# Kernel optimization log

Hardware: AMD Instinct MI355X
Metric: run time of the kernel (lower is better)

## Reference

```python
import jax, jax.numpy as jnp
import numpy as np


def _gelu(x):
    # torch F.gelu default = exact (erf) gelu
    return jax.nn.gelu(x, approximate=False)


def _gatv2(x, src, dst, Wl, bl, Wr, br, att, bout, n):
    """PyG GATv2Conv, concat=False (mean over heads), negative_slope=0.2."""
    H, C = att.shape
    xl = (x @ Wl + bl).reshape(n, H, C)  # source-side transform (messages)
    xr = (x @ Wr + br).reshape(n, H, C)  # target-side transform
    e = jax.nn.leaky_relu(xl[src] + xr[dst], 0.2)      # [E,H,C]
    logits = jnp.einsum('ehc,hc->eh', e, att)          # [E,H]
    # segment softmax over incoming edges of each target node
    m = jax.ops.segment_max(logits, dst, num_segments=n)
    m = jnp.where(jnp.isfinite(m), m, 0.0)
    p = jnp.exp(logits - m[dst])
    den = jax.ops.segment_sum(p, dst, num_segments=n)
    alpha = p / (den[dst] + 1e-16)
    out = jax.ops.segment_sum(alpha[:, :, None] * xl[src], dst, num_segments=n)  # [N,H,C]
    return out.mean(axis=1) + bout


def _gnorm(x, w, b, ms):
    """PyG GraphNorm with a single graph (batch == zeros)."""
    mu = x.mean(axis=0, keepdims=True)
    o = x - ms * mu
    var = (o * o).mean(axis=0, keepdims=True)
    return w * o / jnp.sqrt(var + 1e-5) + b


def setup_inputs() -> dict:
    N, E, HID, LAT = 50000, 300000, 128, 256
    key = jax.random.key(0)
    ks = iter(jax.random.split(key, 48))

    def rn(shape, s=0.05):
        return jax.random.normal(next(ks), shape, jnp.float32) * s

    d = {}
    d['z_g'] = rn((1, LAT), 1.0)
    d['edge_index'] = jax.random.randint(next(ks), (2, E), 0, N, dtype=jnp.int32)
    d['template_vertices'] = rn((N, 3), 1.0)
    d['W_ne1'] = rn((3, HID)); d['b_ne1'] = jnp.zeros((HID,))
    d['W_ne2'] = rn((HID, HID)); d['b_ne2'] = jnp.zeros((HID,))
    d['W_s1'] = rn((LAT, HID)); d['b_s1'] = jnp.zeros((HID,))
    d['W_s2'] = rn((HID, HID)); d['b_s2'] = jnp.zeros((HID,))
    for i, h in ((1, 2), (2, 2), (3, 1)):
        d[f'Wl{i}'] = rn((HID, h * HID)); d[f'bl{i}'] = jnp.zeros((h * HID,))
        d[f'Wr{i}'] = rn((HID, h * HID)); d[f'br{i}'] = jnp.zeros((h * HID,))
        d[f'att{i}'] = rn((h, HID)); d[f'bo{i}'] = jnp.zeros((HID,))
        d[f'gn{i}_w'] = jnp.ones((HID,)); d[f'gn{i}_b'] = jnp.zeros((HID,))
        d[f'gn{i}_ms'] = jnp.ones((HID,))
    d['W_h1'] = rn((HID, HID // 2)); d['b_h1'] = jnp.zeros((HID // 2,))
    d['W_h2'] = rn((HID // 2, 3)); d['b_h2'] = jnp.zeros((3,))
    return d


def reference(z_g, edge_index, template_vertices,
              W_ne1, b_ne1, W_ne2, b_ne2, W_s1, b_s1, W_s2, b_s2,
              Wl1, bl1, Wr1, br1, att1, bo1, gn1_w, gn1_b, gn1_ms,
              Wl2, bl2, Wr2, br2, att2, bo2, gn2_w, gn2_b, gn2_ms,
              Wl3, bl3, Wr3, br3, att3, bo3, gn3_w, gn3_b, gn3_ms,
              W_h1, b_h1, W_h2, b_h2):
    n = template_vertices.shape[0]
    sl = jnp.arange(n, dtype=edge_index.dtype)
    src = jnp.concatenate([edge_index[0], sl])  # GATv2Conv add_self_loops=True
    dst = jnp.concatenate([edge_index[1], sl])
    # node embedding + broadcast style (eval mode -> dropout is identity)
    x = _gelu(template_vertices @ W_ne1 + b_ne1) @ W_ne2 + b_ne2
    style = _gelu(z_g @ W_s1 + b_s1) @ W_s2 + b_s2   # [1, hidden]
    x = x + style
    x = _gelu(_gnorm(_gatv2(x, src, dst, Wl1, bl1, Wr1, br1, att1, bo1, n), gn1_w, gn1_b, gn1_ms))
    x = _gelu(_gnorm(_gatv2(x, src, dst, Wl2, bl2, Wr2, br2, att2, bo2, n), gn2_w, gn2_b, gn2_ms))
    x = _gelu(_gnorm(_gatv2(x, src, dst, Wl3, bl3, Wr3, br3, att3, bo3, n), gn3_w, gn3_b, gn3_ms))
    displacement = _gelu(x @ W_h1 + b_h1) @ W_h2 + b_h2   # [n, 3]
    return displacement
```

## Files before the change

### kernel.cpp

```cpp
#include <hip/hip_runtime.h>
#include <hip/hip_fp16.h>
#include <math.h>

#define DEVINL __device__ __forceinline__

using bf16x8 = __attribute__((ext_vector_type(8))) short;
using f32x4  = __attribute__((ext_vector_type(4))) float;
using u16x4  = __attribute__((ext_vector_type(4))) unsigned short;
using f16x2  = __attribute__((ext_vector_type(2))) _Float16;

DEVINL float gelu_f(float v) { return 0.5f * v * (1.0f + erff(v * 0.7071067811865475f)); }
DEVINL unsigned short f2bf(float f) {
    union { float f; unsigned u; } c; c.f = f;
    unsigned r = c.u + 0x7fffu + ((c.u >> 16) & 1u);
    return (unsigned short)(r >> 16);
}
DEVINL float bf2f(unsigned short s) {
    union { unsigned u; float f; } c; c.u = (unsigned)s << 16;
    return c.f;
}
DEVINL unsigned short f2h(float f) {
    __half h = __float2half_rn(f);
    return *(unsigned short*)&h;
}
DEVINL f16x2 b2h2(unsigned u) {
    union { unsigned u; f16x2 h; } c; c.u = u; return c.h;
}
DEVINL void gl_lds16(const void* g, void* l) {
    __builtin_amdgcn_global_load_lds(
        (const __attribute__((address_space(1))) unsigned*)g,
        (__attribute__((address_space(3))) unsigned*)l, 16, 0, 0);
}

__global__ void style_k(const float* __restrict__ zg, const float* __restrict__ W1,
                        const float* __restrict__ b1, const float* __restrict__ W2,
                        const float* __restrict__ b2, float* __restrict__ style) {
    __shared__ float s1[128];
    int j = threadIdx.x;
    float a = b1[j];
    for (int k = 0; k < 256; k++) a = fmaf(zg[k], W1[k * 128 + j], a);
    s1[j] = gelu_f(a);
    __syncthreads();
    float o = b2[j];
    for (int k = 0; k < 128; k++) o = fmaf(s1[k], W2[k * 128 + j], o);
    style[j] = o;
}

__global__ void ne1_k(const float* __restrict__ tv, const float* __restrict__ W,
                      const float* __restrict__ b, float* __restrict__ h1,
                      int* __restrict__ counts, int Nn) {
    int idx = blockIdx.x * blockDim.x + threadIdx.x;
    if (idx < Nn) counts[idx] = 0;
    if (idx >= Nn * 128) return;
    int n = idx >> 7, c = idx & 127;
    float o = fmaf(tv[n * 3 + 0], W[c],
              fmaf(tv[n * 3 + 1], W[128 + c],
              fmaf(tv[n * 3 + 2], W[256 + c], b[c])));
    h1[idx] = gelu_f(o);
}

struct PrepArgs {
    const float* src[8];
    unsigned short* dst;
    int dstoff[8];
    int off[9];
    int shift[8];
};
__global__ void prep_k(PrepArgs a) {
    int idx = blockIdx.x * 256 + threadIdx.x;
    if (idx >= a.off[8]) return;
    int s = 0;
    while (idx >= a.off[s + 1]) s++;
    int e = idx - a.off[s];
    int sh = a.shift[s];
    int k = e >> sh, j = e & ((1 << sh) - 1);
    float w = a.src[s][e];
    unsigned short hi = f2bf(w);
    unsigned short lo = f2bf(w - bf2f(hi));
    int c = j >> 4, lr = j & 15;
    int s2 = k >> 5, lk = (k >> 3) & 3, i = k & 7;
    int lane = lk * 16 + lr;
    size_t base = (size_t)a.dstoff[s] + (size_t)c * 4096 + s2 * 512 + lane * 8 + i;
    a.dst[base] = hi;
    a.dst[base + 2048] = lo;
}

template <int OUT, int EPI, bool DUAL, typename OutT, int PRE, int SPLIT>
__global__ __launch_bounds__(256) void mfma_lin_k(
    const float* __restrict__ xin,
    const unsigned short* __restrict__ WT0, const float* __restrict__ b0,
    const unsigned short* __restrict__ WT1, const float* __restrict__ b1,
    const float* __restrict__ style, const float* __restrict__ AB,
    OutT* __restrict__ out0, OutT* __restrict__ out1, int Nn) {
    constexpr int CPM = OUT / 16;
    constexpr int NCH = (DUAL ? 2 : 1) * CPM;
    constexpr int CPB = NCH / SPLIT;
    __shared__ uint4 buf[2][512];
    int t = threadIdx.x;
    int wave = t >> 6, lane = t & 63;
    int lr = lane & 15, lk = lane >> 4;
    int base = blockIdx.x * 128 + wave * 32;
    int c0 = blockIdx.y * CPB;
    int r0 = base + lr, r1 = base + 16 + lr;
    int cr0 = min(r0, Nn - 1), cr1 = min(r1, Nn - 1);
    const float* px0 = xin + (size_t)cr0 * 128;
    const float* px1 = xin + (size_t)cr1 * 128;

    bf16x8 xh[2][4], xlo[2][4];
#pragma unroll
    for (int s = 0; s < 4; s++) {
        int cb = s * 32 + lk * 8;
        float A_[8], B_[8];
        if constexpr (PRE == 2) {
            *(f32x4*)&A_[0] = *(const f32x4*)(AB + cb);
            *(f32x4*)&A_[4] = *(const f32x4*)(AB + cb + 4);
            *(f32x4*)&B_[0] = *(const f32x4*)(AB + 128 + cb);
            *(f32x4*)&B_[4] = *(const f32x4*)(AB + 128 + cb + 4);
        }
#pragma unroll
        for (int rr = 0; rr < 2; rr++) {
            const float4* p4 = (const float4*)((rr ? px1 : px0) + cb);
            float4 a = p4[0], b = p4[1];
            float v[8] = {a.x, a.y, a.z, a.w, b.x, b.y, b.z, b.w};
            if constexpr (PRE == 2) {
#pragma unroll
                for (int i = 0; i < 8; i++) v[i] = gelu_f(fmaf(A_[i], v[i], B_[i]));
            }
            bf16x8 h, l;
#pragma unroll
            for (int i = 0; i < 8; i++) {
                unsigned short hb = f2bf(v[i]);
                h[i] = (short)hb;
                l[i] = (short)f2bf(v[i] - bf2f(hb));
            }
            xh[rr][s] = h;
            xlo[rr][s] = l;
        }
    }

    auto stage = [&](int c, int bsel) {
        const unsigned short* Wt = (DUAL && c >= CPM) ? WT1 : WT0;
        int cc = (DUAL && c >= CPM) ? c - CPM : c;
        const char* g = (const char*)(Wt + (size_t)cc * 4096);
        char* l = (char*)&buf[bsel][0];
        gl_lds16(g + t * 16, l + wave * 1024);
        gl_lds16(g + 4096 + t * 16, l + 4096 + wave * 1024);
    };

    stage(c0, 0);
    for (int ci = 0; ci < CPB; ++ci) {
        int c = c0 + ci;
        int cur = ci & 1;
        bool pre = (ci + 1 < CPB);
        if (pre) stage(c + 1, cur ^ 1);
        if (pre) asm volatile("s_waitcnt vmcnt(2)" ::: "memory");
        else     asm volatile("s_waitcnt vmcnt(0)" ::: "memory");
        __builtin_amdgcn_s_barrier();

        int m = (DUAL && c >= CPM) ? 1 : 0;
        int j0 = (c - m * CPM) * 16;
        const float* bias = m ? b1 : b0;
        OutT* out = m ? out1 : out0;
        const bf16x8* W = (const bf16x8*)&buf[cur][0];

        f32x4 acc0 = {0.f, 0.f, 0.f, 0.f}, acc1 = {0.f, 0.f, 0.f, 0.f};
#pragma unroll
        for (int s = 0; s < 4; ++s) {
            bf16x8 wh = W[s * 64 + lane];
            bf16x8 wl = W[256 + s * 64 + lane];
            acc0 = __builtin_amdgcn_mfma_f32_16x16x32_bf16(wh, xh[0][s], acc0, 0, 0, 0);
            acc0 = __builtin_amdgcn_mfma_f32_16x16x32_bf16(wh, xlo[0][s], acc0, 0, 0, 0);
            acc0 = __builtin_amdgcn_mfma_f32_16x16x32_bf16(wl, xh[0][s], acc0, 0, 0, 0);
            acc1 = __builtin_amdgcn_mfma_f32_16x16x32_bf16(wh, xh[1][s], acc1, 0, 0, 0);
            acc1 = __builtin_amdgcn_mfma_f32_16x16x32_bf16(wh, xlo[1][s], acc1, 0, 0, 0);
            acc1 = __builtin_amdgcn_mfma_f32_16x16x32_bf16(wl, xh[1][s], acc1, 0, 0, 0);
        }
        int j = j0 + lk * 4;
        float o0[4], o1[4];
#pragma unroll
        for (int i = 0; i < 4; i++) {
            float bb = bias[j + i];
            if (EPI == 1) bb += style[j + i];
            float v0 = acc0[i] + bb, v1 = acc1[i] + bb;
            if (EPI == 2) { v0 = gelu_f(v0); v1 = gelu_f(v1); }
            o0[i] = v0; o1[i] = v1;
        }
        if constexpr (sizeof(OutT) == 2) {
            u16x4 s0 = {f2h(o0[0]), f2h(o0[1]), f2h(o0[2]), f2h(o0[3])};
            u16x4 s1v = {f2h(o1[0]), f2h(o1[1]), f2h(o1[2]), f2h(o1[3])};
            if (r0 < Nn) *(u16x4*)((unsigned short*)out + (size_t)r0 * OUT + j) = s0;
            if (r1 < Nn) *(u16x4*)((unsigned short*)out + (size_t)r1 * OUT + j) = s1v;
        } else {
            if (r0 < Nn) { f32x4 v = {o0[0], o0[1], o0[2], o0[3]}; *(f32x4*)((float*)out + (size_t)r0 * OUT + j) = v; }
            if (r1 < Nn) { f32x4 v = {o1[0], o1[1], o1[2], o1[3]}; *(f32x4*)((float*)out + (size_t)r1 * OUT + j) = v; }
        }
        __builtin_amdgcn_s_barrier();
    }
}

__global__ void count_k(const int* __restrict__ dst, int* __restrict__ counts, int E, int EP) {
    int e = blockIdx.x * blockDim.x + threadIdx.x;
    if (e >= EP) return;
    int d = (e < E) ? dst[e] : (e - E);
    atomicAdd(&counts[d], 1);
}

__global__ void tile_sum_k(const int* __restrict__ counts, int* __restrict__ tsum, int Nn) {
    int i = blockIdx.x * 256 + threadIdx.x;
    int v = (i < Nn) ? counts[i] : 0;
    int lane = threadIdx.x & 63, wave = threadIdx.x >> 6;
#pragma unroll
    for (int off = 1; off < 64; off <<= 1) v += __shfl_xor(v, off, 64);
    __shared__ int red[4];
    if (lane == 0) red[wave] = v;
    __syncthreads();
    if (threadIdx.x == 0) tsum[blockIdx.x] = red[0] + red[1] + red[2] + red[3];
}

__global__ void tile_scan_k(const int* __restrict__ tsum, int* __restrict__ toff,
                            int ntiles, int* __restrict__ rowptr, int Nn, int total) {
    __shared__ int s[256];
    int t = threadIdx.x;
    int v = (t < ntiles) ? tsum[t] : 0;
    s[t] = v;
    __syncthreads();
    for (int off = 1; off < 256; off <<= 1) {
        int a = (t >= off) ? s[t - off] : 0;
        __syncthreads();
        s[t] += a;
        __syncthreads();
    }
    if (t < ntiles) toff[t] = s[t] - v;
    if (t == 0) rowptr[Nn] = total;
}

__global__ void tile_write_k(const int* __restrict__ counts, const int* __restrict__ toff,
                             int* __restrict__ rowptr, int* __restrict__ fillc, int Nn) {
    int i = blockIdx.x * 256 + threadIdx.x;
    int t = threadIdx.x;
    int v = (i < Nn) ? counts[i] : 0;
    if (i < Nn) fillc[i] = 0;
    __shared__ int s[256];
    s[t] = v;
    __syncthreads();
    for (int off = 1; off < 256; off <<= 1) {
        int a = (t >= off) ? s[t - off] : 0;
        __syncthreads();
        s[t] += a;
        __syncthreads();
    }
    if (i < Nn) rowptr[i] = toff[blockIdx.x] + s[t] - v;
}

__global__ void fill_k(const int* __restrict__ src, const int* __restrict__ dst,
                       const int* __restrict__ rowptr, int* __restrict__ fillc,
                       int* __restrict__ col, int E, int EP) {
    int e = blockIdx.x * blockDim.x + threadIdx.x;
    if (e >= EP) return;
    int d = (e < E) ? dst[e] : (e - E);
    int s = (e < E) ? src[e] : (e - E);
    int pos = atomicAdd(&fillc[d], 1);
    col[rowptr[d] + pos] = s;
}

__global__ __launch_bounds__(256) void gat2_k(
    const unsigned short* __restrict__ xl, const unsigned short* __restrict__ xr,
    const float* __restrict__ att, const float* __restrict__ bo,
    const int* __restrict__ rowptr, const int* __restrict__ col,
    float* __restrict__ y, float* __restrict__ stats, int Nn) {
    if (blockIdx.x == 0 && threadIdx.x < 256) stats[threadIdx.x] = 0.f;
    int n = blockIdx.x * 4 + (threadIdx.x >> 6);
    int lane = threadIdx.x & 63;
    int h = lane >> 5, grp = (lane >> 4) & 1, sub = lane & 15;
    bool act = n < Nn;
    int nn = act ? n : 0;

    uint4 uxr = *(const uint4*)(xr + (size_t)nn * 256 + h * 128 + sub * 8);
    f16x2 xrv[4] = {b2h2(uxr.x), b2h2(uxr.y), b2h2(uxr.z), b2h2(uxr.w)};
    const float* ap = att + h * 128 + sub * 8;
    f16x2 a2[4];
#pragma unroll
    for (int i = 0; i < 4; i++) {
        f16x2 t; t.x = (_Float16)ap[2 * i]; t.y = (_Float16)ap[2 * i + 1];
        a2[i] = t;
    }
    f16x2 c02; c02.x = (_Float16)0.2f; c02.y = (_Float16)0.2f;

    float den = 0.f;
    float acc[8] = {0.f, 0.f, 0.f, 0.f, 0.f, 0.f, 0.f, 0.f};
    int beg = act ? rowptr[n] : 0, endp = act ? rowptr[n + 1] : 0;

    for (int k0 = beg; k0 < endp; k0 += 2) {
        int k = k0 + grp;
        bool ev = k < endp;
        int s = col[ev ? k : beg];
        uint4 u = *(const uint4*)(xl + (size_t)s * 256 + h * 128 + sub * 8);
        f16x2 v2[4] = {b2h2(u.x), b2h2(u.y), b2h2(u.z), b2h2(u.w)};
        float p = 0.f;
#pragma unroll
        for (int i = 0; i < 4; i++) {
            f16x2 t = v2[i] + xrv[i];
            f16x2 e = __builtin_elementwise_max(t, t * c02);
#if __has_builtin(__builtin_amdgcn_fdot2)
            p = __builtin_amdgcn_fdot2(e, a2[i], p, false);
#else
            p = fmaf((float)e.x, (float)a2[i].x, p);
            p = fmaf((float)e.y, (float)a2[i].y, p);
#endif
        }
        p += __shfl_xor(p, 1, 64);
        p += __shfl_xor(p, 2, 64);
        p += __shfl_xor(p, 4, 64);
        p += __shfl_xor(p, 8, 64);
        float pe = ev ? __expf(p) : 0.f;
        den += pe;
#pragma unroll
        for (int i = 0; i < 4; i++) {
            acc[2 * i]     = fmaf(pe, (float)v2[i].x, acc[2 * i]);
            acc[2 * i + 1] = fmaf(pe, (float)v2[i].y, acc[2 * i + 1]);
        }
    }
    den += __shfl_xor(den, 16, 64);
#pragma unroll
    for (int j = 0; j < 8; j++) acc[j] += __shfl_xor(acc[j], 16, 64);
    float inv = 1.0f / (den + 1e-16f);
    float o[8];
#pragma unroll
    for (int j = 0; j < 8; j++) o[j] = acc[j] * inv;
#pragma unroll
    for (int j = 0; j < 8; j++) o[j] = (o[j] + __shfl_xor(o[j], 32, 64)) * 0.5f;
    if (act && lane < 16) {
        const float* bp = bo + sub * 8;
        f32x4 w0 = {o[0] + bp[0], o[1] + bp[1], o[2] + bp[2], o[3] + bp[3]};
        f32x4 w1 = {o[4] + bp[4], o[5] + bp[5], o[6] + bp[6], o[7] + bp[7]};
        *(f32x4*)(y + (size_t)n * 128 + sub * 8) = w0;
        *(f32x4*)(y + (size_t)n * 128 + sub * 8 + 4) = w1;
    }
}

__global__ __launch_bounds__(256) void gat1_k(
    const unsigned short* __restrict__ xl, const unsigned short* __restrict__ xr,
    const float* __restrict__ att, const float* __restrict__ bo,
    const int* __restrict__ rowptr, const int* __restrict__ col,
    float* __restrict__ y, float* __restrict__ stats, int Nn) {
    if (blockIdx.x == 0 && threadIdx.x < 256) stats[threadIdx.x] = 0.f;
    int w = threadIdx.x >> 6;
    int lane = threadIdx.x & 63;
    int g = lane >> 4, sub = lane & 15;
    int n = blockIdx.x * 4 + w;
    bool act = n < Nn;
    int nn = act ? n : 0;

    uint4 uxr = *(const uint4*)(xr + (size_t)nn * 128 + sub * 8);
    f16x2 xrv[4] = {b2h2(uxr.x), b2h2(uxr.y), b2h2(uxr.z), b2h2(uxr.w)};
    const float* ap = att + sub * 8;
    f16x2 a2[4];
#pragma unroll
    for (int i = 0; i < 4; i++) {
        f16x2 t; t.x = (_Float16)ap[2 * i]; t.y = (_Float16)ap[2 * i + 1];
        a2[i] = t;
    }
    f16x2 c02; c02.x = (_Float16)0.2f; c02.y = (_Float16)0.2f;

    float den = 0.f;
    float acc[8] = {0.f, 0.f, 0.f, 0.f, 0.f, 0.f, 0.f, 0.f};
    int beg = act ? rowptr[n] : 0, endp = act ? rowptr[n + 1] : 0;

    for (int k0 = beg; k0 < endp; k0 += 4) {
        int k = k0 + g;
        bool ev = k < endp;
        int s = col[ev ? k : beg];
        uint4 u = *(const uint4*)(xl + (size_t)s * 128 + sub * 8);
        f16x2 v2[4] = {b2h2(u.x), b2h2(u.y), b2h2(u.z), b2h2(u.w)};
        float p = 0.f;
#pragma unroll
        for (int i = 0; i < 4; i++) {
            f16x2 t = v2[i] + xrv[i];
            f16x2 e = __builtin_elementwise_max(t, t * c02);
#if __has_builtin(__builtin_amdgcn_fdot2)
            p = __builtin_amdgcn_fdot2(e, a2[i], p, false);
#else
            p = fmaf((float)e.x, (float)a2[i].x, p);
            p = fmaf((float)e.y, (float)a2[i].y, p);
#endif
        }
        p += __shfl_xor(p, 1, 64);
        p += __shfl_xor(p, 2, 64);
        p += __shfl_xor(p, 4, 64);
        p += __shfl_xor(p, 8, 64);
        float pe = ev ? __expf(p) : 0.f;
        den += pe;
#pragma unroll
        for (int i = 0; i < 4; i++) {
            acc[2 * i]     = fmaf(pe, (float)v2[i].x, acc[2 * i]);
            acc[2 * i + 1] = fmaf(pe, (float)v2[i].y, acc[2 * i + 1]);
        }
    }
#pragma unroll
    for (int off = 16; off <= 32; off <<= 1) {
        den += __shfl_xor(den, off, 64);
#pragma unroll
        for (int j = 0; j < 8; j++) acc[j] += __shfl_xor(acc[j], off, 64);
    }
    float inv = 1.0f / (den + 1e-16f);
    if (act && g == 0) {
        const float* bp = bo + sub * 8;
        f32x4 o0 = {acc[0] * inv + bp[0], acc[1] * inv + bp[1], acc[2] * inv + bp[2], acc[3] * inv + bp[3]};
        f32x4 o1 = {acc[4] * inv + bp[4], acc[5] * inv + bp[5], acc[6] * inv + bp[6], acc[7] * inv + bp[7]};
        *(f32x4*)(y + (size_t)n * 128 + sub * 8) = o0;
        *(f32x4*)(y + (size_t)n * 128 + sub * 8 + 4) = o1;
    }
}

__global__ void gn_stats_k(const float* __restrict__ y, float* __restrict__ stats, int Nn) {
    int c = threadIdx.x;
    int per = (Nn + gridDim.x - 1) / gridDim.x;
    int n0 = blockIdx.x * per, n1 = min(n0 + per, Nn);
    float s = 0.f, s2 = 0.f;
    for (int n = n0; n < n1; n++) {
        float v = y[(size_t)n * 128 + c];
        s += v;
        s2 = fmaf(v, v, s2);
    }
    atomicAdd(&stats[c], s);
    atomicAdd(&stats[128 + c], s2);
}

__global__ void gn_final_k(const float* __restrict__ stats, const float* __restrict__ w,
                           const float* __restrict__ b, const float* __restrict__ ms,
                           float* __restrict__ AB, float invN) {
    int c = threadIdx.x;
    float mu = stats[c] * invN;
    float ex2 = stats[128 + c] * invN;
    float msv = ms[c];
    float var = ex2 - 2.f * msv * mu * mu + msv * msv * mu * mu;
    float r = rsqrtf(var + 1e-5f);
    float A = w[c] * r;
    AB[c] = A;
    AB[128 + c] = b[c] - A * msv * mu;
}

__global__ void head2_k(const float* __restrict__ h, const float* __restrict__ W,
                        const float* __restrict__ b, float* __restrict__ out, int Nn) {
    __shared__ float w[192];
    __shared__ float bb[3];
    int t = threadIdx.x;
    if (t < 192) w[t] = W[t];
    if (t < 3) bb[t] = b[t];
    __syncthreads();
    int n = blockIdx.x * blockDim.x + t;
    if (n >= Nn) return;
    float a0 = bb[0], a1 = bb[1], a2 = bb[2];
    const float4* h4 = reinterpret_cast<const float4*>(h + (size_t)n * 64);
    for (int k4 = 0; k4 < 16; k4++) {
        float4 v = h4[k4];
        int k = k4 * 4;
        a0 = fmaf(v.x, w[(k + 0) * 3 + 0], a0); a1 = fmaf(v.x, w[(k + 0) * 3 + 1], a1); a2 = fmaf(v.x, w[(k + 0) * 3 + 2], a2);
        a0 = fmaf(v.y, w[(k + 1) * 3 + 0], a0); a1 = fmaf(v.y, w[(k + 1) * 3 + 1], a1); a2 = fmaf(v.y, w[(k + 1) * 3 + 2], a2);
        a0 = fmaf(v.z, w[(k + 2) * 3 + 0], a0); a1 = fmaf(v.z, w[(k + 2) * 3 + 1], a1); a2 = fmaf(v.z, w[(k + 2) * 3 + 2], a2);
        a0 = fmaf(v.w, w[(k + 3) * 3 + 0], a0); a1 = fmaf(v.w, w[(k + 3) * 3 + 1], a1); a2 = fmaf(v.w, w[(k + 3) * 3 + 2], a2);
    }
    out[n * 3 + 0] = a0;
    out[n * 3 + 1] = a1;
    out[n * 3 + 2] = a2;
}

extern "C" void kernel_launch(void* const* d_in, const int* in_sizes, int n_in,
                              void* d_out, int out_size, void* d_ws, size_t ws_size,
                              hipStream_t stream) {
    const float* zg = (const float*)d_in[0];
    const int* ei = (const int*)d_in[1];
    const float* tv = (const float*)d_in[2];
    const float* W_ne1 = (const float*)d_in[3];
    const float* b_ne1 = (const float*)d_in[4];
    const float* W_ne2 = (const float*)d_in[5];
    const float* b_ne2 = (const float*)d_in[6];
    const float* W_s1 = (const float*)d_in[7];
    const float* b_s1 = (const float*)d_in[8];
    const float* W_s2 = (const float*)d_in[9];
    const float* b_s2 = (const float*)d_in[10];
    const float *Wl[3], *bl[3], *Wr[3], *br[3], *attp[3], *bop[3], *gnw[3], *gnb[3], *gnms[3];
    for (int L = 0; L < 3; L++) {
        int base = 11 + L * 9;
        Wl[L] = (const float*)d_in[base + 0];
        bl[L] = (const float*)d_in[base + 1];
        Wr[L] = (const float*)d_in[base + 2];
        br[L] = (const float*)d_in[base + 3];
        attp[L] = (const float*)d_in[base + 4];
        bop[L] = (const float*)d_in[base + 5];
        gnw[L] = (const float*)d_in[base + 6];
        gnb[L] = (const float*)d_in[base + 7];
        gnms[L] = (const float*)d_in[base + 8];
    }
    const float* W_h1 = (const float*)d_in[38];
    const float* b_h1 = (const float*)d_in[39];
    const float* W_h2 = (const float*)d_in[40];
    const float* b_h2 = (const float*)d_in[41];

    int E = in_sizes[1] / 2;
    int N = in_sizes[2] / 3;
    int EP = E + N;
    int NT = (N + 255) / 256;
    const int* srcp = ei;
    const int* dstp = ei + E;

    char* p = (char*)d_ws;
    auto alloc = [&](size_t bytes) -> char* {
        char* r = p;
        p += (bytes + 255) & ~(size_t)255;
        return r;
    };
    float* style = (float*)alloc(512);
    float* h1 = (float*)alloc((size_t)N * 128 * 4);
    float* x = (float*)alloc((size_t)N * 128 * 4);
    unsigned short* xle = (unsigned short*)alloc((size_t)N * 256 * 2);
    unsigned short* xre = (unsigned short*)alloc((size_t)N * 256 * 2);
    float* y = (float*)alloc((size_t)N * 128 * 4);
    float* hb = (float*)alloc((size_t)N * 64 * 4);
    float* stats = (float*)alloc(1024);
    float* AB = (float*)alloc(1024);
    int* rowptr = (int*)alloc(((size_t)N + 1) * 4);
    int* counts = (int*)alloc((size_t)N * 4);
    int* fillc = (int*)alloc((size_t)N * 4);
    int* col = (int*)alloc((size_t)EP * 4);
    int* tsum = (int*)alloc((size_t)NT * 4);
    int* toff = (int*)alloc((size_t)NT * 4);
    unsigned short* wt = (unsigned short*)alloc((size_t)376832 * 2);

    PrepArgs pa;
    const float* srcs[8] = {W_ne2, Wl[0], Wr[0], Wl[1], Wr[1], Wl[2], Wr[2], W_h1};
    int outs[8] = {128, 256, 256, 256, 256, 128, 128, 64};
    int off = 0;
    pa.dst = wt;
    for (int s = 0; s < 8; s++) {
        pa.src[s] = srcs[s];
        pa.off[s] = off;
        pa.dstoff[s] = 2 * off;
        pa.shift[s] = (outs[s] == 256) ? 8 : (outs[s] == 128 ? 7 : 6);
        off += 128 * outs[s];
    }
    pa.off[8] = off;
    const unsigned short* ws_ne2 = wt + pa.dstoff[0];
    const unsigned short* ws_l[3] = {wt + pa.dstoff[1], wt + pa.dstoff[3], wt + pa.dstoff[5]};
    const unsigned short* ws_r[3] = {wt + pa.dstoff[2], wt + pa.dstoff[4], wt + pa.dstoff[6]};
    const unsigned short* ws_h1 = wt + pa.dstoff[7];
    prep_k<<<(off + 255) / 256, 256, 0, stream>>>(pa);

    float invN = 1.0f / (float)N;
    int NB = (N + 127) / 128;

    style_k<<<1, 128, 0, stream>>>(zg, W_s1, b_s1, W_s2, b_s2, style);
    ne1_k<<<(N * 128 + 255) / 256, 256, 0, stream>>>(tv, W_ne1, b_ne1, h1, counts, N);
    mfma_lin_k<128, 1, false, float, 0, 1><<<NB, 256, 0, stream>>>(
        h1, ws_ne2, b_ne2, nullptr, nullptr, style, nullptr, x, nullptr, N);

    count_k<<<(EP + 255) / 256, 256, 0, stream>>>(dstp, counts, E, EP);
    tile_sum_k<<<NT, 256, 0, stream>>>(counts, tsum, N);
    tile_scan_k<<<1, 256, 0, stream>>>(tsum, toff, NT, rowptr, N, EP);
    tile_write_k<<<NT, 256, 0, stream>>>(counts, toff, rowptr, fillc, N);
    fill_k<<<(EP + 255) / 256, 256, 0, stream>>>(srcp, dstp, rowptr, fillc, col, E, EP);

    mfma_lin_k<256, 0, true, unsigned short, 0, 2><<<dim3(NB, 2), 256, 0, stream>>>(
        x, ws_l[0], bl[0], ws_r[0], br[0], nullptr, nullptr, xle, xre, N);
    gat2_k<<<(N + 3) / 4, 256, 0, stream>>>(xle, xre, attp[0], bop[0], rowptr, col, y, stats, N);
    gn_stats_k<<<512, 128, 0, stream>>>(y, stats, N);
    gn_final_k<<<1, 128, 0, stream>>>(stats, gnw[0], gnb[0], gnms[0], AB, invN);

    mfma_lin_k<256, 0, true, unsigned short, 2, 2><<<dim3(NB, 2), 256, 0, stream>>>(
        y, ws_l[1], bl[1], ws_r[1], br[1], nullptr, AB, xle, xre, N);
    gat2_k<<<(N + 3) / 4, 256, 0, stream>>>(xle, xre, attp[1], bop[1], rowptr, col, y, stats, N);
    gn_stats_k<<<512, 128, 0, stream>>>(y, stats, N);
    gn_final_k<<<1, 128, 0, stream>>>(stats, gnw[1], gnb[1], gnms[1], AB, invN);

    mfma_lin_k<128, 0, true, unsigned short, 2, 2><<<dim3(NB, 2), 256, 0, stream>>>(
        y, ws_l[2], bl[2], ws_r[2], br[2], nullptr, AB, xle, xre, N);
    gat1_k<<<(N + 3) / 4, 256, 0, stream>>>(xle, xre, attp[2], bop[2], rowptr, col, y, stats, N);
    gn_stats_k<<<512, 128, 0, stream>>>(y, stats, N);
    gn_final_k<<<1, 128, 0, stream>>>(stats, gnw[2], gnb[2], gnms[2], AB, invN);

    mfma_lin_k<64, 2, false, float, 2, 1><<<NB, 256, 0, stream>>>(
        y, ws_h1, b_h1, nullptr, nullptr, nullptr, AB, hb, nullptr, N);
    head2_k<<<(N + 255) / 256, 256, 0, stream>>>(hb, W_h2, b_h2, (float*)d_out, N);
}
```

Measured before the change: 607.1 us.

## Process two weight column chunks per stage and drop the split grid dimension

The MFMA linear kernel now stages and computes two 16-column weight chunks per pipeline step, with a doubled LDS buffer and four accumulators. The blockIdx.y column split is removed, so each block covers every output column for its 128 rows. The goal is to halve the barriers per output and to avoid re-converting the input rows in two separate blocks. In exchange the grid has half as many blocks, and LDS use and register pressure both rise, which may lower occupancy.

Result: faster. 570.5 us (-6.0%).

```diff
diff --git a/kernel.cpp b/kernel.cpp
--- a/kernel.cpp
+++ b/kernel.cpp
@@ -85,7 +85,7 @@
     a.dst[base + 2048] = lo;
 }
 
-template <int OUT, int EPI, bool DUAL, typename OutT, int PRE, int SPLIT>
+template <int OUT, int EPI, bool DUAL, typename OutT, int PRE>
 __global__ __launch_bounds__(256) void mfma_lin_k(
     const float* __restrict__ xin,
     const unsigned short* __restrict__ WT0, const float* __restrict__ b0,
@@ -94,13 +94,12 @@
     OutT* __restrict__ out0, OutT* __restrict__ out1, int Nn) {
     constexpr int CPM = OUT / 16;
     constexpr int NCH = (DUAL ? 2 : 1) * CPM;
-    constexpr int CPB = NCH / SPLIT;
-    __shared__ uint4 buf[2][512];
+    constexpr int NP = NCH / 2;
+    __shared__ uint4 buf[2][1024];
     int t = threadIdx.x;
     int wave = t >> 6, lane = t & 63;
     int lr = lane & 15, lk = lane >> 4;
     int base = blockIdx.x * 128 + wave * 32;
-    int c0 = blockIdx.y * CPB;
     int r0 = base + lr, r1 = base + 16 + lr;
     int cr0 = min(r0, Nn - 1), cr1 = min(r1, Nn - 1);
     const float* px0 = xin + (size_t)cr0 * 128;
@@ -138,61 +137,92 @@
         }
     }
 
-    auto stage = [&](int c, int bsel) {
-        const unsigned short* Wt = (DUAL && c >= CPM) ? WT1 : WT0;
-        int cc = (DUAL && c >= CPM) ? c - CPM : c;
-        const char* g = (const char*)(Wt + (size_t)cc * 4096);
+    auto stagep = [&](int pp, int bsel) {
         char* l = (char*)&buf[bsel][0];
-        gl_lds16(g + t * 16, l + wave * 1024);
-        gl_lds16(g + 4096 + t * 16, l + 4096 + wave * 1024);
+#pragma unroll
+        for (int q = 0; q < 2; q++) {
+            int c = 2 * pp + q;
+            const unsigned short* Wt = (DUAL && c >= CPM) ? WT1 : WT0;
+            int cc = (DUAL && c >= CPM) ? c - CPM : c;
+            const char* g = (const char*)(Wt + (size_t)cc * 4096);
+            gl_lds16(g + t * 16, l + q * 8192 + wave * 1024);
+            gl_lds16(g + 4096 + t * 16, l + q * 8192 + 4096 + wave * 1024);
+        }
     };
 
-    stage(c0, 0);
-    for (int ci = 0; ci < CPB; ++ci) {
-        int c = c0 + ci;
-        int cur = ci & 1;
-        bool pre = (ci + 1 < CPB);
-        if (pre) stage(c + 1, cur ^ 1);
-        if (pre) asm volatile("s_waitcnt vmcnt(2)" ::: "memory");
+    stagep(0, 0);
+    for (int pp = 0; pp < NP; ++pp) {
+        int cur = pp & 1;
+        bool pre = (pp + 1 < NP);
+        if (pre) stagep(pp + 1, cur ^ 1);
+        if (pre) asm volatile("s_waitcnt vmcnt(4)" ::: "memory");
         else     asm volatile("s_waitcnt vmcnt(0)" ::: "memory");
         __builtin_amdgcn_s_barrier();
 
+        int c = 2 * pp;
         int m = (DUAL && c >= CPM) ? 1 : 0;
         int j0 = (c - m * CPM) * 16;
         const float* bias = m ? b1 : b0;
         OutT* out = m ? out1 : out0;
-        const bf16x8* W = (const bf16x8*)&buf[cur][0];
-
-        f32x4 acc0 = {0.f, 0.f, 0.f, 0.f}, acc1 = {0.f, 0.f, 0.f, 0.f};
+        const bf16x8* WA = (const bf16x8*)&buf[cur][0];
+        const bf16x8* WB = (const bf16x8*)&buf[cur][512];
+
+        f32x4 aA0 = {0.f,0.f,0.f,0.f}, aA1 = {0.f,0.f,0.f,0.f};
+        f32x4 aB0 = {0.f,0.f,0.f,0.f}, aB1 = {0.f,0.f,0.f,0.f};
 #pragma unroll
         for (int s = 0; s < 4; ++s) {
-            bf16x8 wh = W[s * 64 + lane];
-            bf16x8 wl = W[256 + s * 64 + lane];
-            acc0 = __builtin_amdgcn_mfma_f32_16x16x32_bf16(wh, xh[0][s], acc0, 0, 0, 0);
-            acc0 = __builtin_amdgcn_mfma_f32_16x16x32_bf16(wh, xlo[0][s], acc0, 0, 0, 0);
-            acc0 = __builtin_amdgcn_mfma_f32_16x16x32_bf16(wl, xh[0][s], acc0, 0, 0, 0);
-            acc1 = __builtin_amdgcn_mfma_f32_16x16x32_bf16(wh, xh[1][s], acc1, 0, 0, 0);
-            acc1 = __builtin_amdgcn_mfma_f32_16x16x32_bf16(wh, xlo[1][s], acc1, 0, 0, 0);
-            acc1 = __builtin_amdgcn_mfma_f32_16x16x32_bf16(wl, xh[1][s], acc1, 0, 0, 0);
-        }
-        int j = j0 + lk * 4;
-        float o0[4], o1[4];
+            bf16x8 whA = WA[s * 64 + lane], wlA = WA[256 + s * 64 + lane];
+            bf16x8 whB = WB[s * 64 + lane], wlB = WB[256 + s * 64 + lane];
+            aA0 = __builtin_amdgcn_mfma_f32_16x16x32_bf16(whA, xh[0][s], aA0, 0, 0, 0);
+            aA0 = __builtin_amdgcn_mfma_f32_16x16x32_bf16(whA, xlo[0][s], aA0, 0, 0, 0);
+            aA0 = __builtin_amdgcn_mfma_f32_16x16x32_bf16(wlA, xh[0][s], aA0, 0, 0, 0);
+            aA1 = __builtin_amdgcn_mfma_f32_16x16x32_bf16(whA, xh[1][s], aA1, 0, 0, 0);
+            aA1 = __builtin_amdgcn_mfma_f32_16x16x32_bf16(whA, xlo[1][s], aA1, 0, 0, 0);
+            aA1 = __builtin_amdgcn_mfma_f32_16x16x32_bf16(wlA, xh[1][s], aA1, 0, 0, 0);
+            aB0 = __builtin_amdgcn_mfma_f32_16x16x32_bf16(whB, xh[0][s], aB0, 0, 0, 0);
+            aB0 = __builtin_amdgcn_mfma_f32_16x16x32_bf16(whB, xlo[0][s], aB0, 0, 0, 0);
+            aB0 = __builtin_amdgcn_mfma_f32_16x16x32_bf16(wlB, xh[0][s], aB0, 0, 0, 0);
+            aB1 = __builtin_amdgcn_mfma_f32_16x16x32_bf16(whB, xh[1][s], aB1, 0, 0, 0);
+            aB1 = __builtin_amdgcn_mfma_f32_16x16x32_bf16(whB, xlo[1][s], aB1, 0, 0, 0);
+            aB1 = __builtin_amdgcn_mfma_f32_16x16x32_bf16(wlB, xh[1][s], aB1, 0, 0, 0);
+        }
+        int jA = j0 + lk * 4, jB = j0 + 16 + lk * 4;
+        float oA0[4], oA1[4], oB0[4], oB1[4];
 #pragma unroll
         for (int i = 0; i < 4; i++) {
-            float bb = bias[j + i];
-            if (EPI == 1) bb += style[j + i];
-            float v0 = acc0[i] + bb, v1 = acc1[i] + bb;
-            if (EPI == 2) { v0 = gelu_f(v0); v1 = gelu_f(v1); }
-            o0[i] = v0; o1[i] = v1;
+            float bA = bias[jA + i], bB = bias[jB + i];
+            if (EPI == 1) { bA += style[jA + i]; bB += style[jB + i]; }
+            float vA0 = aA0[i] + bA, vA1 = aA1[i] + bA;
+            float vB0 = aB0[i] + bB, vB1 = aB1[i] + bB;
+            if (EPI == 2) { vA0 = gelu_f(vA0); vA1 = gelu_f(vA1); vB0 = gelu_f(vB0); vB1 = gelu_f(vB1); }
+            oA0[i] = vA0; oA1[i] = vA1; oB0[i] = vB0; oB1[i] = vB1;
         }
         if constexpr (sizeof(OutT) == 2) {
-            u16x4 s0 = {f2h(o0[0]), f2h(o0[1]), f2h(o0[2]), f2h(o0[3])};
-            u16x4 s1v = {f2h(o1[0]), f2h(o1[1]), f2h(o1[2]), f2h(o1[3])};
-            if (r0 < Nn) *(u16x4*)((unsigned short*)out + (size_t)r0 * OUT + j) = s0;
-            if (r1 < Nn) *(u16x4*)((unsigned short*)out + (size_t)r1 * OUT + j) = s1v;
+            u16x4 sA0 = {f2h(oA0[0]), f2h(oA0[1]), f2h(oA0[2]), f2h(oA0[3])};
+            u16x4 sB0 = {f2h(oB0[0]), f2h(oB0[1]), f2h(oB0[2]), f2h(oB0[3])};
+            u16x4 sA1 = {f2h(oA1[0]), f2h(oA1[1]), f2h(oA1[2]), f2h(oA1[3])};
+            u16x4 sB1 = {f2h(oB1[0]), f2h(oB1[1]), f2h(oB1[2]), f2h(oB1[3])};
+            if (r0 < Nn) {
+                *(u16x4*)((unsigned short*)out + (size_t)r0 * OUT + jA) = sA0;
+                *(u16x4*)((unsigned short*)out + (size_t)r0 * OUT + jB) = sB0;
+            }
+            if (r1 < Nn) {
+                *(u16x4*)((unsigned short*)out + (size_t)r1 * OUT + jA) = sA1;
+                *(u16x4*)((unsigned short*)out + (size_t)r1 * OUT + jB) = sB1;
+            }
         } else {
-            if (r0 < Nn) { f32x4 v = {o0[0], o0[1], o0[2], o0[3]}; *(f32x4*)((float*)out + (size_t)r0 * OUT + j) = v; }
-            if (r1 < Nn) { f32x4 v = {o1[0], o1[1], o1[2], o1[3]}; *(f32x4*)((float*)out + (size_t)r1 * OUT + j) = v; }
+            if (r0 < Nn) {
+                f32x4 vA = {oA0[0], oA0[1], oA0[2], oA0[3]};
+                f32x4 vB = {oB0[0], oB0[1], oB0[2], oB0[3]};
+                *(f32x4*)((float*)out + (size_t)r0 * OUT + jA) = vA;
+                *(f32x4*)((float*)out + (size_t)r0 * OUT + jB) = vB;
+            }
+            if (r1 < Nn) {
+                f32x4 vA = {oA1[0], oA1[1], oA1[2], oA1[3]};
+                f32x4 vB = {oB1[0], oB1[1], oB1[2], oB1[3]};
+                *(f32x4*)((float*)out + (size_t)r1 * OUT + jA) = vA;
+                *(f32x4*)((float*)out + (size_t)r1 * OUT + jB) = vB;
+            }
         }
         __builtin_amdgcn_s_barrier();
     }
@@ -551,7 +581,7 @@
 
     style_k<<<1, 128, 0, stream>>>(zg, W_s1, b_s1, W_s2, b_s2, style);
     ne1_k<<<(N * 128 + 255) / 256, 256, 0, stream>>>(tv, W_ne1, b_ne1, h1, counts, N);
-    mfma_lin_k<128, 1, false, float, 0, 1><<<NB, 256, 0, stream>>>(
+    mfma_lin_k<128, 1, false, float, 0><<<NB, 256, 0, stream>>>(
         h1, ws_ne2, b_ne2, nullptr, nullptr, style, nullptr, x, nullptr, N);
 
     count_k<<<(EP + 255) / 256, 256, 0, stream>>>(dstp, counts, E, EP);
@@ -560,25 +590,25 @@
     tile_write_k<<<NT, 256, 0, stream>>>(counts, toff, rowptr, fillc, N);
     fill_k<<<(EP + 255) / 256, 256, 0, stream>>>(srcp, dstp, rowptr, fillc, col, E, EP);
 
-    mfma_lin_k<256, 0, true, unsigned short, 0, 2><<<dim3(NB, 2), 256, 0, stream>>>(
+    mfma_lin_k<256, 0, true, unsigned short, 0><<<NB, 256, 0, stream>>>(
         x, ws_l[0], bl[0], ws_r[0], br[0], nullptr, nullptr, xle, xre, N);
     gat2_k<<<(N + 3) / 4, 256, 0, stream>>>(xle, xre, attp[0], bop[0], rowptr, col, y, stats, N);
     gn_stats_k<<<512, 128, 0, stream>>>(y, stats, N);
     gn_final_k<<<1, 128, 0, stream>>>(stats, gnw[0], gnb[0], gnms[0], AB, invN);
 
-    mfma_lin_k<256, 0, true, unsigned short, 2, 2><<<dim3(NB, 2), 256, 0, stream>>>(
+    mfma_lin_k<256, 0, true, unsigned short, 2><<<NB, 256, 0, stream>>>(
         y, ws_l[1], bl[1], ws_r[1], br[1], nullptr, AB, xle, xre, N);
     gat2_k<<<(N + 3) / 4, 256, 0, stream>>>(xle, xre, attp[1], bop[1], rowptr, col, y, stats, N);
     gn_stats_k<<<512, 128, 0, stream>>>(y, stats, N);
     gn_final_k<<<1, 128, 0, stream>>>(stats, gnw[1], gnb[1], gnms[1], AB, invN);
 
-    mfma_lin_k<128, 0, true, unsigned short, 2, 2><<<dim3(NB, 2), 256, 0, stream>>>(
+    mfma_lin_k<128, 0, true, unsigned short, 2><<<NB, 256, 0, stream>>>(
         y, ws_l[2], bl[2], ws_r[2], br[2], nullptr, AB, xle, xre, N);
     gat1_k<<<(N + 3) / 4, 256, 0, stream>>>(xle, xre, attp[2], bop[2], rowptr, col, y, stats, N);
     gn_stats_k<<<512, 128, 0, stream>>>(y, stats, N);
     gn_final_k<<<1, 128, 0, stream>>>(stats, gnw[2], gnb[2], gnms[2], AB, invN);
 
-    mfma_lin_k<64, 2, false, float, 2, 1><<<NB, 256, 0, stream>>>(
+    mfma_lin_k<64, 2, false, float, 2><<<NB, 256, 0, stream>>>(
         y, ws_h1, b_h1, nullptr, nullptr, nullptr, AB, hb, nullptr, N);
     head2_k<<<(N + 255) / 256, 256, 0, stream>>>(hb, W_h2, b_h2, (float*)d_out, N);
 }
```
